# Kernel tuning notes

Measured on AMD Instinct MI355X. Metric: run time of the kernel, lower is better.

The kernel has to match this reference:

```python
import jax, jax.numpy as jnp
import numpy as np

B, S, D = 2, 2048, 768
NH, GH = 12, 4
HD = D // NH            # 64
GD = HD * GH            # 256 (grouped KV projection width)
REP = NH // GH          # 3  (repeat factor for KV heads)
SCALE = HD ** -0.5
MASK_FILL = -1e-09      # faithful to the original (NOT -1e9)


def setup_inputs() -> dict:
    key = jax.random.key(0)
    ks = jax.random.split(key, 9)
    init = 0.02
    x = jax.random.normal(ks[0], (B, S, D), dtype=jnp.float32)
    masks = jnp.tril(jnp.ones((S, S), dtype=jnp.float32)) > 0  # bool causal mask
    Wq = jax.random.normal(ks[1], (D, D), dtype=jnp.float32) * init
    bq = jnp.zeros((D,), dtype=jnp.float32)
    Wk = jax.random.normal(ks[2], (D, GD), dtype=jnp.float32) * init
    bk = jnp.zeros((GD,), dtype=jnp.float32)
    Wv = jax.random.normal(ks[3], (D, GD), dtype=jnp.float32) * init
    bv = jnp.zeros((GD,), dtype=jnp.float32)
    Wo = jax.random.normal(ks[4], (D, D), dtype=jnp.float32) * init
    bo = jnp.zeros((D,), dtype=jnp.float32)
    return {"x": x, "masks": masks, "Wq": Wq, "bq": bq, "Wk": Wk, "bk": bk,
            "Wv": Wv, "bv": bv, "Wo": Wo, "bo": bo}


def reference(x, masks, Wq, bq, Wk, bk, Wv, bv, Wo, bo):
    bs, seq, _ = x.shape
    # projections (weights stored [in, out])
    q = (x @ Wq + bq).reshape(bs, seq, NH, HD).transpose(0, 2, 1, 3)   # [b, nh, s, hd]
    k = (x @ Wk + bk).reshape(bs, seq, GH, HD).transpose(0, 2, 1, 3)   # [b, gh, s, hd]
    v = (x @ Wv + bv).reshape(bs, seq, GH, HD).transpose(0, 2, 1, 3)
    # repeat_interleave KV heads to match query heads (faithful to original)
    k = jnp.repeat(k, REP, axis=1)                                     # [b, nh, s, hd]
    v = jnp.repeat(v, REP, axis=1)
    scores = jnp.einsum('bhqd,bhkd->bhqk', q, k) * SCALE               # [b, nh, s, s]
    # original: masked_fill(masks == 0, -1e-09)
    scores = jnp.where(masks, scores, MASK_FILL)
    attn = jax.nn.softmax(scores, axis=-1)
    out = jnp.einsum('bhqk,bhkd->bhqd', attn, v)                       # [b, nh, s, hd]
    # faithful to original buggy merge: transpose(-1,-2).contiguous().view(b, s, dim)
    out = out.transpose(0, 1, 3, 2).reshape(bs, seq, D)
    return out @ Wo + bo
```

## Files before the change

### kernel.cpp

```cpp
#include <hip/hip_runtime.h>
#include <stdint.h>


typedef unsigned short ushort_t;
typedef short bf16x8 __attribute__((ext_vector_type(8)));
typedef float f32x4 __attribute__((ext_vector_type(4)));

#define MFMA(a, b, c) __builtin_amdgcn_mfma_f32_16x16x32_bf16((a), (b), (c), 0, 0, 0)

__device__ __forceinline__ ushort_t f2bf(float f) {
    union { float f; unsigned u; } v; v.f = f;
    const unsigned r = v.u + 0x7FFFu + ((v.u >> 16) & 1u);
    return (ushort_t)(r >> 16);
}

__device__ __forceinline__ void lds_barrier() {
    asm volatile("s_waitcnt lgkmcnt(0)" ::: "memory");
    __builtin_amdgcn_s_barrier();
    __builtin_amdgcn_sched_barrier(0);
}

__global__ __launch_bounds__(256) void prep_kernel(
    const float* __restrict__ x, ushort_t* __restrict__ xb,
    const float* __restrict__ Wq, const float* __restrict__ Wk,
    const float* __restrict__ Wv, const float* __restrict__ Wo,
    ushort_t* __restrict__ WqT, ushort_t* __restrict__ WkT,
    ushort_t* __restrict__ WvT, ushort_t* __restrict__ WoT) {
    const int bid = blockIdx.x;
    const int tid = threadIdx.x;
    if (bid < 3072) {
        const int i = (bid * 256 + tid) * 4;
        const float4 v = *(const float4*)(x + i);
        uint2 p;
        p.x = (unsigned)f2bf(v.x) | ((unsigned)f2bf(v.y) << 16);
        p.y = (unsigned)f2bf(v.z) | ((unsigned)f2bf(v.w) << 16);
        *(uint2*)(xb + i) = p;
        return;
    }
    const int rem = bid - 3072;
    const int z = rem / 144;
    const int rem2 = rem % 144;
    const int kxt = rem2 / 12, nyt = rem2 % 12;
    const float* src; ushort_t* dst; int N;
    if (z == 0)      { src = Wq; dst = WqT; N = 768; }
    else if (z == 1) { src = Wk; dst = WkT; N = 256; }
    else if (z == 2) { src = Wv; dst = WvT; N = 256; }
    else             { src = Wo; dst = WoT; N = 768; }
    const int k0 = kxt * 64, n0 = nyt * 64;
    if (n0 >= N) return;

    __shared__ float Ts[64][65];
    const int r = tid >> 2, cb = (tid & 3) * 16;
    #pragma unroll
    for (int jj = 0; jj < 4; ++jj) {
        const float4 v = *(const float4*)(src + (k0 + r) * N + n0 + cb + jj * 4);
        Ts[cb + jj * 4 + 0][r] = v.x; Ts[cb + jj * 4 + 1][r] = v.y;
        Ts[cb + jj * 4 + 2][r] = v.z; Ts[cb + jj * 4 + 3][r] = v.w;
    }
    __syncthreads();
    const int n = tid >> 2, kc = (tid & 3) * 16;
    unsigned hbuf[16];
    #pragma unroll
    for (int j = 0; j < 16; ++j) hbuf[j] = f2bf(Ts[n][kc + j]);
    uint4 p0, p1;
    p0.x = hbuf[0] | (hbuf[1] << 16);   p0.y = hbuf[2] | (hbuf[3] << 16);
    p0.z = hbuf[4] | (hbuf[5] << 16);   p0.w = hbuf[6] | (hbuf[7] << 16);
    p1.x = hbuf[8] | (hbuf[9] << 16);   p1.y = hbuf[10] | (hbuf[11] << 16);
    p1.z = hbuf[12] | (hbuf[13] << 16); p1.w = hbuf[14] | (hbuf[15] << 16);
    *(uint4*)(dst + (n0 + n) * 768 + k0 + kc) = p0;
    *(uint4*)(dst + (n0 + n) * 768 + k0 + kc + 8) = p1;
}

__global__ __launch_bounds__(512) void qkv_kernel(
    const ushort_t* __restrict__ xb,
    const ushort_t* __restrict__ WqT, const ushort_t* __restrict__ WkT,
    const ushort_t* __restrict__ WvT,
    const float* __restrict__ bq, const float* __restrict__ bk,
    const float* __restrict__ bv,
    ushort_t* __restrict__ Qb, ushort_t* __restrict__ Kb,
    ushort_t* __restrict__ Vtb) {
    const int ct = blockIdx.x, rt = blockIdx.y;
    const int r0 = rt * 128;
    const ushort_t* WT; const float* bias; int head; int kind;
    if (ct < 12)      { WT = WqT; bias = bq; head = ct;      kind = 0; }
    else if (ct < 16) { WT = WkT; bias = bk; head = ct - 12; kind = 1; }
    else              { WT = WvT; bias = bv; head = ct - 16; kind = 2; }
    const int n0 = head * 64;

    __shared__ uint4 Xs[1024];
    __shared__ uint4 Ws[512];

    const int tid = threadIdx.x;
    const int lane = tid & 63, w = tid >> 6;
    const int quad = lane >> 4, l15 = lane & 15;
    const int srx = tid >> 2, sbx = (tid & 3) * 2;
    const int srw = tid >> 3, sbw = tid & 7;

    f32x4 acc[4] = {{0,0,0,0},{0,0,0,0},{0,0,0,0},{0,0,0,0}};

    for (int k0 = 0; k0 < 768; k0 += 64) {
        __syncthreads();
        #pragma unroll
        for (int c = 0; c < 2; ++c) {
            const int blk = sbx + c;
            Xs[srx * 8 + (blk ^ (srx & 7))] = *(const uint4*)(xb + (r0 + srx) * 768 + k0 + blk * 8);
        }
        Ws[srw * 8 + (sbw ^ (srw & 7))] = *(const uint4*)(WT + (n0 + srw) * 768 + k0 + sbw * 8);
        __syncthreads();
        #pragma unroll
        for (int ks = 0; ks < 2; ++ks) {
            const int arow = 16 * w + l15;
            const bf16x8 af = *(const bf16x8*)&Xs[arow * 8 + ((quad + 4 * ks) ^ (arow & 7))];
            #pragma unroll
            for (int ctt = 0; ctt < 4; ++ctt) {
                const int brow = 16 * ctt + l15;
                const bf16x8 bfr = *(const bf16x8*)&Ws[brow * 8 + ((quad + 4 * ks) ^ (brow & 7))];
                acc[ctt] = MFMA(af, bfr, acc[ctt]);
            }
        }
    }
    #pragma unroll
    for (int ctt = 0; ctt < 4; ++ctt) {
        const int cd = ctt * 16 + l15;
        const float bv_ = bias[n0 + cd];
        const int row0 = r0 + 16 * w + quad * 4;
        const int b = row0 >> 11;
        if (kind == 2) {
            const int s0 = row0 & 2047;
            unsigned h[4];
            #pragma unroll
            for (int reg = 0; reg < 4; ++reg) h[reg] = f2bf(acc[ctt][reg] + bv_);
            uint2 pk; pk.x = h[0] | (h[1] << 16); pk.y = h[2] | (h[3] << 16);
            *(uint2*)(Vtb + ((b * 4 + head) * 64 + cd) * 2048 + s0) = pk;
        } else {
            #pragma unroll
            for (int reg = 0; reg < 4; ++reg) {
                const int row = row0 + reg;
                const int s = row & 2047;
                const float pre = acc[ctt][reg] + bv_;
                const ushort_t hh = f2bf((kind == 0) ? pre * 0.125f : pre);
                if (kind == 0) Qb[((b * 12 + head) * 2048 + s) * 64 + cd] = hh;
                else           Kb[((b * 4 + head) * 2048 + s) * 64 + cd] = hh;
            }
        }
    }
}

__global__ __launch_bounds__(256) void v_suffix_kernel(
    const ushort_t* __restrict__ Vtb, float* __restrict__ SV) {
    const int b = blockIdx.z, g = blockIdx.y, d0 = blockIdx.x * 8;
    const int tid = threadIdx.x;
    const int dd = tid >> 5, tt = tid & 31;
    const ushort_t* vp = Vtb + ((b * 4 + g) * 64 + d0 + dd) * 2048 + tt * 64;
    float s = 0.f;
    #pragma unroll
    for (int j = 0; j < 8; ++j) {
        const bf16x8 v = *(const bf16x8*)(vp + j * 8);
        #pragma unroll
        for (int e = 0; e < 8; ++e) {
            union { unsigned u; float f; } c;
            c.u = ((unsigned)(ushort_t)v[e]) << 16;
            s += c.f;
        }
    }
    __shared__ float cs[8][32];
    cs[dd][tt] = s;
    __syncthreads();
    if (tid < 8) {
        float run = 0.f;
        const int base = ((b * 4 + g) * 32) * 64 + d0 + tid;
        for (int j = 31; j >= 0; --j) {
            run += cs[tid][j];
            SV[base + j * 64] = run;
        }
    }
}

__global__ __launch_bounds__(256) void attn_kernel(
    const ushort_t* __restrict__ Qb, const ushort_t* __restrict__ Kb,
    const ushort_t* __restrict__ Vtb, const float* __restrict__ SV,
    ushort_t* __restrict__ aT_hi, ushort_t* __restrict__ aT_lo) {
    const int hb = blockIdx.x;
    const int h = hb % 12, b = hb / 12;
    const int qt = 31 - (int)blockIdx.y;
    const int g = h / 3;
    const int q0 = qt * 64;
    const int nt = qt + 1;
    const int tid = threadIdx.x;
    const int lane = tid & 63, w = tid >> 6;
    const int quad = lane >> 4, l15 = lane & 15;

    __shared__ uint4 K_l[2][512];
    __shared__ uint4 V_l[2][512];
    __shared__ __align__(16) ushort_t P_l[64 * 72];

    const ushort_t* Qp = Qb + ((b * 12 + h) * 2048 + q0 + 16 * w + l15) * 64;
    const bf16x8 qf0 = *(const bf16x8*)(Qp + quad * 8);
    const bf16x8 qf1 = *(const bf16x8*)(Qp + 32 + quad * 8);

    const ushort_t* Kp = Kb + (b * 4 + g) * 2048 * 64;
    const ushort_t* Vp = Vtb + (b * 4 + g) * 64 * 2048;

    f32x4 o[4] = {{0,0,0,0},{0,0,0,0},{0,0,0,0},{0,0,0,0}};
    float lacc[4] = {0.f, 0.f, 0.f, 0.f};

    const int sr = tid >> 2, sb = (tid & 3) * 2;
    const int qg = q0 + 16 * w + quad * 4;
    const int prow = (16 * w + quad * 4) * 72;

    uint4 rK[2], rV[2];
    auto issue_loads = [&](int t) {
        const int k0 = t * 64;
        #pragma unroll
        for (int c = 0; c < 2; ++c) {
            const int blk = sb + c;
            rK[c] = *(const uint4*)(Kp + (k0 + sr) * 64 + blk * 8);
            rV[c] = *(const uint4*)(Vp + sr * 2048 + k0 + blk * 8);
        }
    };
    auto write_lds = [&](int buf) {
        #pragma unroll
        for (int c = 0; c < 2; ++c) {
            const int blk = sb + c;
            K_l[buf][sr * 8 + (blk ^ (sr & 7))] = rK[c];
            V_l[buf][sr * 8 + (blk ^ (sr & 7))] = rV[c];
        }
    };
    auto compute = [&](int t, int buf, bool diag) {
        const int k0 = t * 64;
        #pragma unroll
        for (int ctt = 0; ctt < 4; ++ctt) {
            const int key = ctt * 16 + l15;
            f32x4 s = {0, 0, 0, 0};
            s = MFMA(qf0, *(const bf16x8*)&K_l[buf][key * 8 + ((quad + 0) ^ (key & 7))], s);
            s = MFMA(qf1, *(const bf16x8*)&K_l[buf][key * 8 + ((quad + 4) ^ (key & 7))], s);
            if (diag) {
                const int kg = k0 + key;
                #pragma unroll
                for (int reg = 0; reg < 4; ++reg) {
                    float e = __expf(s[reg]);
                    e = (kg <= qg + reg) ? e : 1.0f;
                    lacc[reg] += e;
                    P_l[prow + reg * 72 + key] = f2bf(e);
                }
            } else {
                #pragma unroll
                for (int reg = 0; reg < 4; ++reg) {
                    const float e = __expf(s[reg]);
                    lacc[reg] += e;
                    P_l[prow + reg * 72 + key] = f2bf(e);
                }
            }
        }
        const bf16x8 pf0 = *(const bf16x8*)&P_l[(16 * w + l15) * 72 + quad * 8];
        const bf16x8 pf1 = *(const bf16x8*)&P_l[(16 * w + l15) * 72 + 32 + quad * 8];
        #pragma unroll
        for (int ctt = 0; ctt < 4; ++ctt) {
            const int d = ctt * 16 + l15;
            o[ctt] = MFMA(pf0, *(const bf16x8*)&V_l[buf][d * 8 + ((quad + 0) ^ (d & 7))], o[ctt]);
            o[ctt] = MFMA(pf1, *(const bf16x8*)&V_l[buf][d * 8 + ((quad + 4) ^ (d & 7))], o[ctt]);
        }
    };

    issue_loads(0);
    write_lds(0);
    if (nt > 1) issue_loads(1);
    lds_barrier();
    for (int t = 0; t < nt; ++t) {
        if (t + 1 < nt) {
            write_lds((t + 1) & 1);
            if (t + 2 < nt) issue_loads(t + 2);
        }
        compute(t, t & 1, t == nt - 1);
        lds_barrier();
    }

    if (qt < 31) {
        const float* svp = SV + ((b * 4 + g) * 32 + qt + 1) * 64;
        #pragma unroll
        for (int ctt = 0; ctt < 4; ++ctt) {
            const float t = svp[ctt * 16 + l15];
            #pragma unroll
            for (int reg = 0; reg < 4; ++reg) o[ctt][reg] += t;
        }
    }
    const float tailc = (float)(2048 - 64 - q0);

    #pragma unroll
    for (int reg = 0; reg < 4; ++reg) {
        float v = lacc[reg];
        v += __shfl_xor(v, 1); v += __shfl_xor(v, 2);
        v += __shfl_xor(v, 4); v += __shfl_xor(v, 8);
        lacc[reg] = 1.f / (v + tailc);
    }
    const int t0 = q0 + 16 * w + quad * 4;
    #pragma unroll
    for (int ctt = 0; ctt < 4; ++ctt) {
        const int d = ctt * 16 + l15;
        unsigned hh[4], hl[4];
        #pragma unroll
        for (int reg = 0; reg < 4; ++reg) {
            const float val = o[ctt][reg] * lacc[reg];
            const ushort_t hi = f2bf(val);
            union { unsigned u; float f; } vv; vv.u = (unsigned)hi << 16;
            hh[reg] = hi;
            hl[reg] = f2bf(val - vv.f);
        }
        const int idx = (b * 768 + h * 64 + d) * 2048 + t0;
        uint2 ph, pl;
        ph.x = hh[0] | (hh[1] << 16); ph.y = hh[2] | (hh[3] << 16);
        pl.x = hl[0] | (hl[1] << 16); pl.y = hl[2] | (hl[3] << 16);
        *(uint2*)(aT_hi + idx) = ph;
        *(uint2*)(aT_lo + idx) = pl;
    }
}

__global__ __launch_bounds__(512) void out_proj_kernel(
    const ushort_t* __restrict__ aT_hi, const ushort_t* __restrict__ aT_lo,
    const ushort_t* __restrict__ WoT, const float* __restrict__ bo,
    float* __restrict__ out) {
    const int ct = blockIdx.x, rt = blockIdx.y;
    const int r0 = rt * 128, c0 = ct * 64;
    __shared__ uint4 Ah[1024];
    __shared__ uint4 Al[1024];
    __shared__ uint4 Ws[512];
    const int tid = threadIdx.x;
    const int lane = tid & 63, w = tid >> 6;
    const int quad = lane >> 4, l15 = lane & 15;
    const int srx = tid >> 2, sbx = (tid & 3) * 2;
    const int srw = tid >> 3, sbw = tid & 7;

    f32x4 acc[4] = {{0,0,0,0},{0,0,0,0},{0,0,0,0},{0,0,0,0}};

    for (int k0 = 0; k0 < 768; k0 += 64) {
        __syncthreads();
        #pragma unroll
        for (int c = 0; c < 2; ++c) {
            const int blk = sbx + c;
            const int slot = srx * 8 + (blk ^ (srx & 7));
            Ah[slot] = *(const uint4*)(aT_hi + (r0 + srx) * 768 + k0 + blk * 8);
            Al[slot] = *(const uint4*)(aT_lo + (r0 + srx) * 768 + k0 + blk * 8);
        }
        Ws[srw * 8 + (sbw ^ (srw & 7))] = *(const uint4*)(WoT + (c0 + srw) * 768 + k0 + sbw * 8);
        __syncthreads();
        #pragma unroll
        for (int ks = 0; ks < 2; ++ks) {
            const int arow = 16 * w + l15;
            const int aslot = arow * 8 + ((quad + 4 * ks) ^ (arow & 7));
            const bf16x8 ah = *(const bf16x8*)&Ah[aslot];
            const bf16x8 al = *(const bf16x8*)&Al[aslot];
            #pragma unroll
            for (int ctt = 0; ctt < 4; ++ctt) {
                const int brow = 16 * ctt + l15;
                const bf16x8 bfr = *(const bf16x8*)&Ws[brow * 8 + ((quad + 4 * ks) ^ (brow & 7))];
                acc[ctt] = MFMA(ah, bfr, acc[ctt]);
                acc[ctt] = MFMA(al, bfr, acc[ctt]);
            }
        }
    }
    #pragma unroll
    for (int ctt = 0; ctt < 4; ++ctt) {
        const int cd = c0 + ctt * 16 + l15;
        const float bo_v = bo[cd];
        #pragma unroll
        for (int reg = 0; reg < 4; ++reg) {
            const int row = r0 + 16 * w + quad * 4 + reg;
            out[row * 768 + cd] = acc[ctt][reg] + bo_v;
        }
    }
}

extern "C" void kernel_launch(void* const* d_in, const int* in_sizes, int n_in,
                              void* d_out, int out_size, void* d_ws, size_t ws_size,
                              hipStream_t stream) {
    const float* x  = (const float*)d_in[0];
    const float* Wq = (const float*)d_in[2];
    const float* bq = (const float*)d_in[3];
    const float* Wk = (const float*)d_in[4];
    const float* bk = (const float*)d_in[5];
    const float* Wv = (const float*)d_in[6];
    const float* bv = (const float*)d_in[7];
    const float* Wo = (const float*)d_in[8];
    const float* bo = (const float*)d_in[9];
    float* out = (float*)d_out;

    uint8_t* wsb = (uint8_t*)d_ws;
    ushort_t* xb    = (ushort_t*)(wsb);
    ushort_t* WqT   = (ushort_t*)(wsb + 6291456);
    ushort_t* WkT   = (ushort_t*)(wsb + 7471104);
    ushort_t* WvT   = (ushort_t*)(wsb + 7864320);
    ushort_t* WoT   = (ushort_t*)(wsb + 8257536);
    ushort_t* Qb    = (ushort_t*)(wsb + 9437184);
    ushort_t* Kb    = (ushort_t*)(wsb + 15728640);
    ushort_t* Vtb   = (ushort_t*)(wsb + 17825792);
    ushort_t* aT_hi = (ushort_t*)(wsb + 19922944);
    ushort_t* aT_lo = (ushort_t*)(wsb + 26214400);
    float* SV = (float*)wsb;

    prep_kernel<<<3648, 256, 0, stream>>>(x, xb, Wq, Wk, Wv, Wo, WqT, WkT, WvT, WoT);
    qkv_kernel<<<dim3(20, 32), 512, 0, stream>>>(xb, WqT, WkT, WvT, bq, bk, bv, Qb, Kb, Vtb);
    v_suffix_kernel<<<dim3(8, 4, 2), 256, 0, stream>>>(Vtb, SV);
    attn_kernel<<<dim3(24, 32), 256, 0, stream>>>(Qb, Kb, Vtb, SV, aT_hi, aT_lo);
    out_proj_kernel<<<dim3(12, 32), 512, 0, stream>>>(aT_hi, aT_lo, WoT, bo, out);
}
```

Baseline: 212.2 us.

## Double-buffer GEMM LDS tiles with direct global-to-LDS async loads

The QKV and output projection GEMMs now use two LDS buffers and global_load_lds to copy tiles straight from global memory into LDS, prefetching the next K-slice while MFMAs run on the current one. This removes the register round trip and one barrier per iteration. The output projection also handles the hi and lo split of the activations as 24 sequential K-steps over one A buffer, instead of loading both per step. LDS use doubles, and correctness depends on the swizzled per-lane layout matching what global_load_lds writes and on the barrier covering async completion.

Measured after the change: 206.9 us. -2.5%, faster.

```diff
diff --git a/kernel.cpp b/kernel.cpp
--- a/kernel.cpp
+++ b/kernel.cpp
@@ -12,6 +12,12 @@
     union { float f; unsigned u; } v; v.f = f;
     const unsigned r = v.u + 0x7FFFu + ((v.u >> 16) & 1u);
     return (ushort_t)(r >> 16);
+}
+
+__device__ __forceinline__ void gload_lds16(const void* g, void* l) {
+    __builtin_amdgcn_global_load_lds(
+        (const __attribute__((address_space(1))) void*)g,
+        (__attribute__((address_space(3))) void*)l, 16, 0, 0);
 }
 
 __device__ __forceinline__ void lds_barrier() {
@@ -87,37 +93,44 @@
     else              { WT = WvT; bias = bv; head = ct - 16; kind = 2; }
     const int n0 = head * 64;
 
-    __shared__ uint4 Xs[1024];
-    __shared__ uint4 Ws[512];
+    __shared__ uint4 Xs[2][1024];
+    __shared__ uint4 Ws[2][512];
 
     const int tid = threadIdx.x;
     const int lane = tid & 63, w = tid >> 6;
     const int quad = lane >> 4, l15 = lane & 15;
-    const int srx = tid >> 2, sbx = (tid & 3) * 2;
-    const int srw = tid >> 3, sbw = tid & 7;
+    const int lrow = lane >> 3;
+    const int lblk = (lane & 7) ^ (lrow & 7);
+
+    const ushort_t* xg0 = xb + (r0 + 16 * w + lrow) * 768 + lblk * 8;
+    const ushort_t* xg1 = xg0 + 8 * 768;
+    const ushort_t* wg  = WT + (n0 + 8 * w + lrow) * 768 + lblk * 8;
 
     f32x4 acc[4] = {{0,0,0,0},{0,0,0,0},{0,0,0,0},{0,0,0,0}};
 
-    for (int k0 = 0; k0 < 768; k0 += 64) {
-        __syncthreads();
-        #pragma unroll
-        for (int c = 0; c < 2; ++c) {
-            const int blk = sbx + c;
-            Xs[srx * 8 + (blk ^ (srx & 7))] = *(const uint4*)(xb + (r0 + srx) * 768 + k0 + blk * 8);
-        }
-        Ws[srw * 8 + (sbw ^ (srw & 7))] = *(const uint4*)(WT + (n0 + srw) * 768 + k0 + sbw * 8);
-        __syncthreads();
-        #pragma unroll
-        for (int ks = 0; ks < 2; ++ks) {
+    auto stage = [&](int buf, int k0) {
+        gload_lds16(xg0 + k0, &Xs[buf][128 * w]);
+        gload_lds16(xg1 + k0, &Xs[buf][128 * w + 64]);
+        gload_lds16(wg + k0, &Ws[buf][64 * w]);
+    };
+
+    stage(0, 0);
+    __syncthreads();
+    for (int ks = 0; ks < 12; ++ks) {
+        const int buf = ks & 1;
+        if (ks + 1 < 12) stage(buf ^ 1, (ks + 1) * 64);
+        #pragma unroll
+        for (int k2 = 0; k2 < 2; ++k2) {
             const int arow = 16 * w + l15;
-            const bf16x8 af = *(const bf16x8*)&Xs[arow * 8 + ((quad + 4 * ks) ^ (arow & 7))];
+            const bf16x8 af = *(const bf16x8*)&Xs[buf][arow * 8 + ((quad + 4 * k2) ^ (arow & 7))];
             #pragma unroll
             for (int ctt = 0; ctt < 4; ++ctt) {
                 const int brow = 16 * ctt + l15;
-                const bf16x8 bfr = *(const bf16x8*)&Ws[brow * 8 + ((quad + 4 * ks) ^ (brow & 7))];
+                const bf16x8 bfr = *(const bf16x8*)&Ws[buf][brow * 8 + ((quad + 4 * k2) ^ (brow & 7))];
                 acc[ctt] = MFMA(af, bfr, acc[ctt]);
             }
         }
+        __syncthreads();
     }
     #pragma unroll
     for (int ctt = 0; ctt < 4; ++ctt) {
@@ -321,42 +334,44 @@
     float* __restrict__ out) {
     const int ct = blockIdx.x, rt = blockIdx.y;
     const int r0 = rt * 128, c0 = ct * 64;
-    __shared__ uint4 Ah[1024];
-    __shared__ uint4 Al[1024];
-    __shared__ uint4 Ws[512];
+    __shared__ uint4 As[2][1024];
+    __shared__ uint4 Ws[2][512];
     const int tid = threadIdx.x;
     const int lane = tid & 63, w = tid >> 6;
     const int quad = lane >> 4, l15 = lane & 15;
-    const int srx = tid >> 2, sbx = (tid & 3) * 2;
-    const int srw = tid >> 3, sbw = tid & 7;
+    const int lrow = lane >> 3;
+    const int lblk = (lane & 7) ^ (lrow & 7);
+
+    const int aoff = (r0 + 16 * w + lrow) * 768 + lblk * 8;
+    const ushort_t* wg = WoT + (c0 + 8 * w + lrow) * 768 + lblk * 8;
 
     f32x4 acc[4] = {{0,0,0,0},{0,0,0,0},{0,0,0,0},{0,0,0,0}};
 
-    for (int k0 = 0; k0 < 768; k0 += 64) {
-        __syncthreads();
-        #pragma unroll
-        for (int c = 0; c < 2; ++c) {
-            const int blk = sbx + c;
-            const int slot = srx * 8 + (blk ^ (srx & 7));
-            Ah[slot] = *(const uint4*)(aT_hi + (r0 + srx) * 768 + k0 + blk * 8);
-            Al[slot] = *(const uint4*)(aT_lo + (r0 + srx) * 768 + k0 + blk * 8);
-        }
-        Ws[srw * 8 + (sbw ^ (srw & 7))] = *(const uint4*)(WoT + (c0 + srw) * 768 + k0 + sbw * 8);
-        __syncthreads();
-        #pragma unroll
-        for (int ks = 0; ks < 2; ++ks) {
+    auto stage = [&](int buf, int ks) {
+        const ushort_t* Ab = (ks < 12 ? aT_hi : aT_lo);
+        const int k0 = (ks < 12 ? ks : ks - 12) * 64;
+        gload_lds16(Ab + aoff + k0, &As[buf][128 * w]);
+        gload_lds16(Ab + aoff + 8 * 768 + k0, &As[buf][128 * w + 64]);
+        gload_lds16(wg + k0, &Ws[buf][64 * w]);
+    };
+
+    stage(0, 0);
+    __syncthreads();
+    for (int ks = 0; ks < 24; ++ks) {
+        const int buf = ks & 1;
+        if (ks + 1 < 24) stage(buf ^ 1, ks + 1);
+        #pragma unroll
+        for (int k2 = 0; k2 < 2; ++k2) {
             const int arow = 16 * w + l15;
-            const int aslot = arow * 8 + ((quad + 4 * ks) ^ (arow & 7));
-            const bf16x8 ah = *(const bf16x8*)&Ah[aslot];
-            const bf16x8 al = *(const bf16x8*)&Al[aslot];
+            const bf16x8 af = *(const bf16x8*)&As[buf][arow * 8 + ((quad + 4 * k2) ^ (arow & 7))];
             #pragma unroll
             for (int ctt = 0; ctt < 4; ++ctt) {
                 const int brow = 16 * ctt + l15;
-                const bf16x8 bfr = *(const bf16x8*)&Ws[brow * 8 + ((quad + 4 * ks) ^ (brow & 7))];
-                acc[ctt] = MFMA(ah, bfr, acc[ctt]);
-                acc[ctt] = MFMA(al, bfr, acc[ctt]);
+                const bf16x8 bfr = *(const bf16x8*)&Ws[buf][brow * 8 + ((quad + 4 * k2) ^ (brow & 7))];
+                acc[ctt] = MFMA(af, bfr, acc[ctt]);
             }
         }
+        __syncthreads();
     }
     #pragma unroll
     for (int ctt = 0; ctt < 4; ++ctt) {
```
